# Optimization experiments

Hardware: AMD Instinct MI355X
Metric: run time of the kernel (lower is better)

## Reference

```python
import jax, jax.numpy as jnp
import numpy as np

TEMPERATURE = 0.1


def setup_inputs() -> dict:
    key = jax.random.key(0)
    k1, k2 = jax.random.split(key)
    N, D = 8192, 128
    features = jax.random.normal(k1, (N, D), dtype=jnp.float32)
    labels = jax.random.randint(k2, (N,), 0, 1000, dtype=jnp.int64)
    return {"features": features, "labels": labels}


def reference(features, labels):
    N = features.shape[0]
    # L2-normalize rows
    feats = features / jnp.linalg.norm(features, axis=1, keepdims=True)
    # positive-pair mask from labels [N, N]
    labels = labels.reshape(-1, 1)
    mask = (labels == labels.T).astype(feats.dtype)
    # similarity matrix scaled by temperature
    sim = jnp.matmul(feats, feats.T) / TEMPERATURE
    # exclude self-comparisons (diagonal)
    logits_mask = 1.0 - jnp.eye(N, dtype=feats.dtype)
    mask = mask * logits_mask
    exp_logits = jnp.exp(sim) * logits_mask
    log_prob = sim - jnp.log(exp_logits.sum(axis=1, keepdims=True) + 1e-9)
    mask_sum = mask.sum(axis=1)
    mask_sum = jnp.where(mask_sum == 0, jnp.ones_like(mask_sum), mask_sum)
    mean_log_prob_pos = (mask * log_prob).sum(axis=1) / mask_sum
    return -mean_log_prob_pos.mean()
```

## Files before the change

kernel.cpp:

```cpp
#include <hip/hip_runtime.h>
#include <hip/hip_bf16.h>
#include <math.h>


constexpr int N = 8192;
constexpr int D = 128;

typedef __attribute__((ext_vector_type(8))) short short8;
typedef __attribute__((ext_vector_type(4))) float f32x4;

__device__ __forceinline__ float fast_exp2(float x) {
#if __has_builtin(__builtin_amdgcn_exp2f)
    return __builtin_amdgcn_exp2f(x);
#else
    return __expf(x * 0.69314718056f);
#endif
}

__device__ __forceinline__ void gload_lds16(const void* g, void* s) {
    __builtin_amdgcn_global_load_lds(
        (const __attribute__((address_space(1))) unsigned int*)g,
        (__attribute__((address_space(3))) unsigned int*)s, 16, 0, 0);
}

__device__ __forceinline__ void stage_tile(const unsigned short* __restrict__ src,
                                           unsigned short* dst, int row0,
                                           int w, int lr, int lq) {
#pragma unroll
    for (int it = 0; it < 8; ++it) {
        int rbase = w * 32 + it * 4;
        int r = rbase + lr;
        int q = lq ^ (r & 7);
        gload_lds16(src + ((size_t)(row0 + r) * D + q * 8), dst + rbase * D);
    }
}

__global__ void zero_kernel(int* __restrict__ hist) {
    hist[threadIdx.x] = 0;
}

__global__ void prep_kernel(const float* __restrict__ F,
                            const int* __restrict__ labels,
                            unsigned short* __restrict__ Fb,
                            float* __restrict__ rowExp,
                            float* __restrict__ rowPos,
                            int* __restrict__ hist) {
    int row = blockIdx.x * 4 + (threadIdx.x >> 6);
    int l = threadIdx.x & 63;
    float2 v = ((const float2*)(F + (size_t)row * D))[l];
    float ss = v.x * v.x + v.y * v.y;
#pragma unroll
    for (int off = 32; off > 0; off >>= 1) ss += __shfl_xor(ss, off);
    float sc = sqrtf(14.4269504089f / ss);
    __hip_bfloat16 hx = __float2bfloat16(v.x * sc);
    __hip_bfloat16 hy = __float2bfloat16(v.y * sc);
    ushort2 u;
    u.x = *(unsigned short*)&hx;
    u.y = *(unsigned short*)&hy;
    ((ushort2*)(Fb + (size_t)row * D))[l] = u;
    if (l == 0) {
        rowExp[row] = 0.0f;
        rowPos[row] = 0.0f;
        atomicAdd(&hist[labels[row]], 1);
    }
}

__global__ __launch_bounds__(256, 2) void sim_kernel(
    const unsigned short* __restrict__ Fb, const int* __restrict__ labels,
    float* __restrict__ rowExp, float* __restrict__ rowPos) {
    __shared__ unsigned short At[128 * D];
    __shared__ unsigned short Bt[128 * D];

    int bid = blockIdx.x, q = 0, base = 0;
    while (bid >= base + 4 * (16 - q)) { base += 4 * (16 - q); ++q; }
    int rem = bid - base, ng = 16 - q;
    int ti = 4 * q + rem / ng;
    int g = 15 - (rem % ng);
    int tjs = max(ti, 4 * g), tje = 4 * g + 3;
    const int i0 = ti * 128;

    const int t = threadIdx.x, w = t >> 6, l = t & 63;
    const int lr = l >> 4, lq = l & 15;
    const int c = l & 15, quad = l >> 4;
    const int wy = w >> 1, wx = w & 1;

    stage_tile(Fb, At, i0, w, lr, lq);
    stage_tile(Fb, Bt, tjs * 128, w, lr, lq);

    int li[4][4];
#pragma unroll
    for (int m = 0; m < 4; ++m)
#pragma unroll
        for (int r = 0; r < 4; ++r)
            li[m][r] = labels[i0 + wy * 64 + m * 16 + quad * 4 + r];

    float RE[4][4] = {}, RP[4][4] = {};

    for (int tj = tjs; tj <= tje; ++tj) {
        __syncthreads();
        int j0 = tj * 128;
        f32x4 acc[4][4] = {};
#pragma unroll
        for (int kk = 0; kk < 4; ++kk) {
            short8 af[4], bf[4];
            int sl = (kk * 4 + quad) ^ (c & 7);
#pragma unroll
            for (int m = 0; m < 4; ++m) {
                af[m] = *(const short8*)&At[(wy * 64 + m * 16 + c) * D + sl * 8];
                bf[m] = *(const short8*)&Bt[(wx * 64 + m * 16 + c) * D + sl * 8];
            }
#pragma unroll
            for (int m = 0; m < 4; ++m)
#pragma unroll
                for (int n = 0; n < 4; ++n)
                    acc[m][n] = __builtin_amdgcn_mfma_f32_16x16x32_bf16(
                        af[m], bf[n], acc[m][n], 0, 0, 0);
        }
        __syncthreads();
        if (tj < tje) stage_tile(Fb, Bt, (tj + 1) * 128, w, lr, lq);

        int lj[4];
#pragma unroll
        for (int n = 0; n < 4; ++n) lj[n] = labels[j0 + wx * 64 + n * 16 + c];
        const bool diag = (tj == ti);
        float ce[4] = {}, cp[4] = {};
#pragma unroll
        for (int m = 0; m < 4; ++m) {
#pragma unroll
            for (int n = 0; n < 4; ++n) {
#pragma unroll
                for (int r = 0; r < 4; ++r) {
                    float s2 = acc[m][n][r];
                    bool self = diag && ((wy * 64 + m * 16 + quad * 4 + r) ==
                                         (wx * 64 + n * 16 + c));
                    float e = self ? 0.0f : fast_exp2(s2);
                    float p = (!self && li[m][r] == lj[n]) ? s2 : 0.0f;
                    RE[m][r] += e;
                    RP[m][r] += p;
                    ce[n] += e;
                    cp[n] += p;
                }
            }
        }
        if (!diag) {
#pragma unroll
            for (int n = 0; n < 4; ++n) {
                ce[n] += __shfl_xor(ce[n], 16);
                ce[n] += __shfl_xor(ce[n], 32);
                cp[n] += __shfl_xor(cp[n], 16);
                cp[n] += __shfl_xor(cp[n], 32);
            }
            if (quad == 0) {
#pragma unroll
                for (int n = 0; n < 4; ++n) {
                    int gj = j0 + wx * 64 + n * 16 + c;
                    atomicAdd(&rowExp[gj], ce[n]);
                    atomicAdd(&rowPos[gj], cp[n]);
                }
            }
        }
    }

#pragma unroll
    for (int m = 0; m < 4; ++m)
#pragma unroll
        for (int r = 0; r < 4; ++r) {
#pragma unroll
            for (int off = 1; off < 16; off <<= 1) {
                RE[m][r] += __shfl_xor(RE[m][r], off);
                RP[m][r] += __shfl_xor(RP[m][r], off);
            }
        }
    if (c == 0) {
#pragma unroll
        for (int m = 0; m < 4; ++m)
#pragma unroll
            for (int r = 0; r < 4; ++r) {
                int gi = i0 + wy * 64 + m * 16 + quad * 4 + r;
                atomicAdd(&rowExp[gi], RE[m][r]);
                atomicAdd(&rowPos[gi], RP[m][r]);
            }
    }
}

__global__ void finalize_kernel(const float* __restrict__ rowExp,
                                const float* __restrict__ rowPos,
                                const int* __restrict__ labels,
                                const int* __restrict__ hist,
                                float* __restrict__ out) {
    int t = threadIdx.x;
    float a = 0.0f;
    for (int i = t; i < N; i += 1024) {
        int cnt = hist[labels[i]] - 1;
        if (cnt > 0)
            a += logf(rowExp[i] + 1e-9f) -
                 0.69314718056f * rowPos[i] / (float)cnt;
    }
#pragma unroll
    for (int off = 32; off > 0; off >>= 1) a += __shfl_xor(a, off);
    __shared__ float ws16[16];
    if ((t & 63) == 0) ws16[t >> 6] = a;
    __syncthreads();
    if (t == 0) {
        float s = 0.0f;
#pragma unroll
        for (int i = 0; i < 16; ++i) s += ws16[i];
        out[0] = s / (float)N;
    }
}

extern "C" void kernel_launch(void* const* d_in, const int* in_sizes, int n_in,
                              void* d_out, int out_size, void* d_ws, size_t ws_size,
                              hipStream_t stream) {
    const float* F      = (const float*)d_in[0];
    const int*   labels = (const int*)d_in[1];
    float* out = (float*)d_out;

    unsigned short* Fb = (unsigned short*)d_ws;
    float* rowExp = (float*)(Fb + (size_t)N * D);
    float* rowPos = rowExp + N;
    int*   hist   = (int*)(rowPos + N);

    zero_kernel<<<1, 1024, 0, stream>>>(hist);
    prep_kernel<<<N / 4, 256, 0, stream>>>(F, labels, Fb, rowExp, rowPos, hist);
    sim_kernel<<<544, 256, 0, stream>>>(Fb, labels, rowExp, rowPos);
    finalize_kernel<<<1, 1024, 0, stream>>>(rowExp, rowPos, labels, hist, out);
}
```

Measured before the change: 103.7 us.

## Use 512-thread blocks, rebalance tile schedule, count positives in sim kernel

Doubles the sim kernel's block size to 8 waves, each computing a 32x64 sub-tile, and raises launch bounds to 4 blocks per CU. The tile scheduler is reworked so diagonal tile groups run as separate shorter blocks after the off-diagonal blocks. The label histogram and zero kernel are removed: positive counts are now accumulated with atomics inside the sim kernel, which drops one launch but adds a third accumulator and more atomics. Label loads are hoisted ahead of the barrier, and finalize switches to a fast log.

```diff
diff --git a/kernel.cpp b/kernel.cpp
--- a/kernel.cpp
+++ b/kernel.cpp
@@ -23,28 +23,11 @@
         (__attribute__((address_space(3))) unsigned int*)s, 16, 0, 0);
 }
 
-__device__ __forceinline__ void stage_tile(const unsigned short* __restrict__ src,
-                                           unsigned short* dst, int row0,
-                                           int w, int lr, int lq) {
-#pragma unroll
-    for (int it = 0; it < 8; ++it) {
-        int rbase = w * 32 + it * 4;
-        int r = rbase + lr;
-        int q = lq ^ (r & 7);
-        gload_lds16(src + ((size_t)(row0 + r) * D + q * 8), dst + rbase * D);
-    }
-}
-
-__global__ void zero_kernel(int* __restrict__ hist) {
-    hist[threadIdx.x] = 0;
-}
-
 __global__ void prep_kernel(const float* __restrict__ F,
-                            const int* __restrict__ labels,
                             unsigned short* __restrict__ Fb,
                             float* __restrict__ rowExp,
                             float* __restrict__ rowPos,
-                            int* __restrict__ hist) {
+                            float* __restrict__ rowCnt) {
     int row = blockIdx.x * 4 + (threadIdx.x >> 6);
     int l = threadIdx.x & 63;
     float2 v = ((const float2*)(F + (size_t)row * D))[l];
@@ -61,56 +44,80 @@
     if (l == 0) {
         rowExp[row] = 0.0f;
         rowPos[row] = 0.0f;
-        atomicAdd(&hist[labels[row]], 1);
-    }
-}
-
-__global__ __launch_bounds__(256, 2) void sim_kernel(
+        rowCnt[row] = 0.0f;
+    }
+}
+
+__device__ __forceinline__ void stage_tile(const unsigned short* __restrict__ src,
+                                           unsigned short* dst, int row0,
+                                           int w, int lr, int lq) {
+#pragma unroll
+    for (int it = 0; it < 4; ++it) {
+        int rbase = w * 16 + it * 4;
+        int r = rbase + lr;
+        int q = lq ^ (r & 7);
+        gload_lds16(src + ((size_t)(row0 + r) * D + q * 8), dst + rbase * D);
+    }
+}
+
+__global__ __launch_bounds__(512, 4) void sim_kernel(
     const unsigned short* __restrict__ Fb, const int* __restrict__ labels,
-    float* __restrict__ rowExp, float* __restrict__ rowPos) {
+    float* __restrict__ rowExp, float* __restrict__ rowPos,
+    float* __restrict__ rowCnt) {
     __shared__ unsigned short At[128 * D];
     __shared__ unsigned short Bt[128 * D];
 
-    int bid = blockIdx.x, q = 0, base = 0;
-    while (bid >= base + 4 * (16 - q)) { base += 4 * (16 - q); ++q; }
-    int rem = bid - base, ng = 16 - q;
-    int ti = 4 * q + rem / ng;
-    int g = 15 - (rem % ng);
-    int tjs = max(ti, 4 * g), tje = 4 * g + 3;
+    int bid = blockIdx.x;
+    int ti, tjs, tje;
+    if (bid < 480) {
+        int q = 0, base = 0;
+        while (bid >= base + 4 * (15 - q)) { base += 4 * (15 - q); ++q; }
+        int rem = bid - base, ng = 15 - q;
+        ti = 4 * q + rem / ng;
+        int g = q + 1 + (rem % ng);
+        tjs = 4 * g; tje = 4 * g + 3;
+    } else if (bid < 496) { ti = (bid - 480) * 4;     tjs = ti; tje = ti + 3; }
+    else if (bid < 512)   { ti = (bid - 496) * 4 + 1; tjs = ti; tje = ti + 2; }
+    else if (bid < 528)   { ti = (bid - 512) * 4 + 2; tjs = ti; tje = ti + 1; }
+    else                  { ti = (bid - 528) * 4 + 3; tjs = ti; tje = ti; }
     const int i0 = ti * 128;
 
     const int t = threadIdx.x, w = t >> 6, l = t & 63;
     const int lr = l >> 4, lq = l & 15;
     const int c = l & 15, quad = l >> 4;
-    const int wy = w >> 1, wx = w & 1;
+    const int wy = w & 3, wx = w >> 2;
 
     stage_tile(Fb, At, i0, w, lr, lq);
     stage_tile(Fb, Bt, tjs * 128, w, lr, lq);
 
-    int li[4][4];
-#pragma unroll
-    for (int m = 0; m < 4; ++m)
+    int li[2][4];
+#pragma unroll
+    for (int m = 0; m < 2; ++m)
 #pragma unroll
         for (int r = 0; r < 4; ++r)
-            li[m][r] = labels[i0 + wy * 64 + m * 16 + quad * 4 + r];
-
-    float RE[4][4] = {}, RP[4][4] = {};
+            li[m][r] = labels[i0 + wy * 32 + m * 16 + quad * 4 + r];
+
+    float RE[2][4] = {}, RP[2][4] = {}, RC[2][4] = {};
 
     for (int tj = tjs; tj <= tje; ++tj) {
+        int j0 = tj * 128;
+        int lj[4];
+#pragma unroll
+        for (int n = 0; n < 4; ++n) lj[n] = labels[j0 + wx * 64 + n * 16 + c];
         __syncthreads();
-        int j0 = tj * 128;
-        f32x4 acc[4][4] = {};
+        f32x4 acc[2][4] = {};
 #pragma unroll
         for (int kk = 0; kk < 4; ++kk) {
-            short8 af[4], bf[4];
             int sl = (kk * 4 + quad) ^ (c & 7);
-#pragma unroll
-            for (int m = 0; m < 4; ++m) {
-                af[m] = *(const short8*)&At[(wy * 64 + m * 16 + c) * D + sl * 8];
-                bf[m] = *(const short8*)&Bt[(wx * 64 + m * 16 + c) * D + sl * 8];
-            }
-#pragma unroll
-            for (int m = 0; m < 4; ++m)
+            short8 af[2], bf[4];
+#pragma unroll
+            for (int m = 0; m < 2; ++m)
+                af[m] = *(const short8*)&At[(wy * 32 + m * 16 + c) * D + sl * 8];
+#pragma unroll
+            for (int n = 0; n < 4; ++n)
+                bf[n] = *(const short8*)&Bt[(wx * 64 + n * 16 + c) * D + sl * 8];
+#pragma unroll
+            for (int m = 0; m < 2; ++m)
 #pragma unroll
                 for (int n = 0; n < 4; ++n)
                     acc[m][n] = __builtin_amdgcn_mfma_f32_16x16x32_bf16(
@@ -119,36 +126,32 @@
         __syncthreads();
         if (tj < tje) stage_tile(Fb, Bt, (tj + 1) * 128, w, lr, lq);
 
-        int lj[4];
-#pragma unroll
-        for (int n = 0; n < 4; ++n) lj[n] = labels[j0 + wx * 64 + n * 16 + c];
         const bool diag = (tj == ti);
-        float ce[4] = {}, cp[4] = {};
-#pragma unroll
-        for (int m = 0; m < 4; ++m) {
+        float ce[4] = {}, cp[4] = {}, cc[4] = {};
+#pragma unroll
+        for (int m = 0; m < 2; ++m) {
 #pragma unroll
             for (int n = 0; n < 4; ++n) {
 #pragma unroll
                 for (int r = 0; r < 4; ++r) {
                     float s2 = acc[m][n][r];
-                    bool self = diag && ((wy * 64 + m * 16 + quad * 4 + r) ==
+                    bool self = diag && ((wy * 32 + m * 16 + quad * 4 + r) ==
                                          (wx * 64 + n * 16 + c));
+                    bool pos = (li[m][r] == lj[n]) && !self;
                     float e = self ? 0.0f : fast_exp2(s2);
-                    float p = (!self && li[m][r] == lj[n]) ? s2 : 0.0f;
-                    RE[m][r] += e;
-                    RP[m][r] += p;
-                    ce[n] += e;
-                    cp[n] += p;
+                    float p = pos ? s2 : 0.0f;
+                    float o = pos ? 1.0f : 0.0f;
+                    RE[m][r] += e; RP[m][r] += p; RC[m][r] += o;
+                    ce[n] += e;    cp[n] += p;    cc[n] += o;
                 }
             }
         }
         if (!diag) {
 #pragma unroll
             for (int n = 0; n < 4; ++n) {
-                ce[n] += __shfl_xor(ce[n], 16);
-                ce[n] += __shfl_xor(ce[n], 32);
-                cp[n] += __shfl_xor(cp[n], 16);
-                cp[n] += __shfl_xor(cp[n], 32);
+                ce[n] += __shfl_xor(ce[n], 16); ce[n] += __shfl_xor(ce[n], 32);
+                cp[n] += __shfl_xor(cp[n], 16); cp[n] += __shfl_xor(cp[n], 32);
+                cc[n] += __shfl_xor(cc[n], 16); cc[n] += __shfl_xor(cc[n], 32);
             }
             if (quad == 0) {
 #pragma unroll
@@ -156,45 +159,47 @@
                     int gj = j0 + wx * 64 + n * 16 + c;
                     atomicAdd(&rowExp[gj], ce[n]);
                     atomicAdd(&rowPos[gj], cp[n]);
+                    atomicAdd(&rowCnt[gj], cc[n]);
                 }
             }
         }
     }
 
 #pragma unroll
-    for (int m = 0; m < 4; ++m)
+    for (int m = 0; m < 2; ++m)
 #pragma unroll
         for (int r = 0; r < 4; ++r) {
 #pragma unroll
             for (int off = 1; off < 16; off <<= 1) {
                 RE[m][r] += __shfl_xor(RE[m][r], off);
                 RP[m][r] += __shfl_xor(RP[m][r], off);
+                RC[m][r] += __shfl_xor(RC[m][r], off);
             }
         }
     if (c == 0) {
 #pragma unroll
-        for (int m = 0; m < 4; ++m)
+        for (int m = 0; m < 2; ++m)
 #pragma unroll
             for (int r = 0; r < 4; ++r) {
-                int gi = i0 + wy * 64 + m * 16 + quad * 4 + r;
+                int gi = i0 + wy * 32 + m * 16 + quad * 4 + r;
                 atomicAdd(&rowExp[gi], RE[m][r]);
                 atomicAdd(&rowPos[gi], RP[m][r]);
+                atomicAdd(&rowCnt[gi], RC[m][r]);
             }
     }
 }
 
 __global__ void finalize_kernel(const float* __restrict__ rowExp,
                                 const float* __restrict__ rowPos,
-                                const int* __restrict__ labels,
-                                const int* __restrict__ hist,
+                                const float* __restrict__ rowCnt,
                                 float* __restrict__ out) {
     int t = threadIdx.x;
     float a = 0.0f;
     for (int i = t; i < N; i += 1024) {
-        int cnt = hist[labels[i]] - 1;
-        if (cnt > 0)
-            a += logf(rowExp[i] + 1e-9f) -
-                 0.69314718056f * rowPos[i] / (float)cnt;
+        float cnt = rowCnt[i];
+        if (cnt > 0.5f)
+            a += __logf(rowExp[i] + 1e-9f) -
+                 0.69314718056f * rowPos[i] / cnt;
     }
 #pragma unroll
     for (int off = 32; off > 0; off >>= 1) a += __shfl_xor(a, off);
@@ -219,10 +224,9 @@
     unsigned short* Fb = (unsigned short*)d_ws;
     float* rowExp = (float*)(Fb + (size_t)N * D);
     float* rowPos = rowExp + N;
-    int*   hist   = (int*)(rowPos + N);
-
-    zero_kernel<<<1, 1024, 0, stream>>>(hist);
-    prep_kernel<<<N / 4, 256, 0, stream>>>(F, labels, Fb, rowExp, rowPos, hist);
-    sim_kernel<<<544, 256, 0, stream>>>(Fb, labels, rowExp, rowPos);
-    finalize_kernel<<<1, 1024, 0, stream>>>(rowExp, rowPos, labels, hist, out);
-}
+    float* rowCnt = rowPos + N;
+
+    prep_kernel<<<N / 4, 256, 0, stream>>>(F, Fb, rowExp, rowPos, rowCnt);
+    sim_kernel<<<544, 512, 0, stream>>>(Fb, labels, rowExp, rowPos, rowCnt);
+    finalize_kernel<<<1, 1024, 0, stream>>>(rowExp, rowPos, rowCnt, out);
+}
```

Result: slower. 140.0 us (+35.0%).
